# Kernel tuning notes

Hardware: AMD Instinct MI355X
Metric: run time of the kernel (lower is better)

Reference implementation:

```python
import jax, jax.numpy as jnp
import numpy as np
import math

NH, DH, BS, LOCAL, RAND, NCLS = 12, 64, 49, 3, 3, 1
WINDOW = (8, 14, 14)
NKV = LOCAL + RAND


def make_rel_pos_index():
    ws = WINDOW
    rel_size = [2 * w - 1 for w in ws]
    coords = np.stack(np.meshgrid(*[np.arange(w) for w in ws], indexing='ij')).reshape(len(ws), -1)
    rel = (coords[:, :, None] - coords[:, None, :]).transpose(1, 2, 0).astype(np.int64)
    for i, w in enumerate(ws):
        rel[:, :, i] += w - 1
    for i, r in enumerate(rel_size[1:]):
        rel[:, :, :i + 1] *= r
    n = coords.shape[1]
    S = n + NCLS
    idx = np.zeros((S, S), dtype=np.int64)
    idx[NCLS:, NCLS:] = rel.sum(-1)
    start = int(np.prod(rel_size))
    idx[:NCLS, NCLS:] = np.arange(NCLS)[:, None] + start
    start += NCLS
    idx[NCLS:, :NCLS] = np.arange(NCLS)[None, :] + start
    start += NCLS
    idx[:NCLS, :NCLS] = np.arange(NCLS ** 2).reshape(NCLS, NCLS) + start
    return idx.astype(np.int32)


def setup_inputs() -> dict:
    key = jax.random.key(0)
    ks = jax.random.split(key, 8)
    B, S, D = 8, 1569, 768
    M = (S - NCLS) // BS  # 32 blocks
    hidden_states = jax.random.normal(ks[0], (B, S, D), dtype=jnp.float32)
    Wq = jax.random.normal(ks[1], (D, D), dtype=jnp.float32) * 0.02
    bq = jax.random.normal(ks[2], (D,), dtype=jnp.float32) * 0.02
    Wk = jax.random.normal(ks[3], (D, D), dtype=jnp.float32) * 0.02
    Wv = jax.random.normal(ks[4], (D, D), dtype=jnp.float32) * 0.02
    bv = jax.random.normal(ks[5], (D,), dtype=jnp.float32) * 0.02
    rel_table = jax.random.normal(ks[6], (10938, NH), dtype=jnp.float32) * 0.02
    rel_pos_index = jnp.asarray(make_rel_pos_index())
    rand_idx = jnp.sort(jax.random.randint(ks[7], (M, RAND), 0, M), axis=1).astype(jnp.int32)
    return {"hidden_states": hidden_states, "Wq": Wq, "bq": bq, "Wk": Wk, "Wv": Wv,
            "bv": bv, "rel_table": rel_table, "rel_pos_index": rel_pos_index, "rand_idx": rand_idx}


def reference(hidden_states, Wq, bq, Wk, Wv, bv, rel_table, rel_pos_index, rand_idx):
    B, S, D = hidden_states.shape
    scale = 1.0 / math.sqrt(DH)
    q = hidden_states @ Wq + bq
    k = hidden_states @ Wk          # key has no bias in BeitSelfAttention
    v = hidden_states @ Wv + bv
    split = lambda x: x.reshape(B, S, NH, DH).transpose(0, 2, 1, 3)  # b h s d
    q, k, v = split(q), split(k), split(v)

    # --- dense attention for cls queries over all keys ---
    cls_q = q[:, :, :NCLS]
    sim_cls = jnp.einsum('bhid,bhjd->bhij', cls_q, k) * scale
    bias_cls = rel_table[rel_pos_index[:NCLS, :]]           # [ncls, S, H]
    sim_cls = sim_cls + bias_cls.transpose(2, 0, 1)[None]
    attn_cls = jax.nn.softmax(sim_cls, axis=-1)
    out_cls = jnp.einsum('bhij,bhjd->bhid', attn_cls, v)    # [B,H,ncls,DH]

    # --- block-sparse attention for local queries ---
    loc_q = q[:, :, NCLS:]
    cls_k, loc_k = k[:, :, :NCLS], k[:, :, NCLS:]
    cls_v, loc_v = v[:, :, :NCLS], v[:, :, NCLS:]
    N = S - NCLS
    M = N // BS  # evenly divisible -> pad_q = 0
    qb = loc_q.reshape(B, NH, M, BS, DH)
    kb = loc_k.reshape(B, NH, M, BS, DH)
    vb = loc_v.reshape(B, NH, M, BS, DH)

    # local + random key-block indices per query block: [M, NKV]
    offs = jnp.arange(-(LOCAL // 2), LOCAL // 2 + 1)
    local_idx = (jnp.arange(M)[:, None] + offs[None, :]) % M
    attn_idx = jnp.concatenate([local_idx.astype(jnp.int32), rand_idx], axis=1)

    kg = kb[:, :, attn_idx]   # [B,H,M,NKV,BS,DH]
    vg = vb[:, :, attn_idx]

    sim_loc = jnp.einsum('bhmid,bhmnjd->bhminj', qb, kg).reshape(B, NH, M, BS, NKV * BS)
    sim_c = jnp.einsum('bhmid,bhjd->bhmij', qb, cls_k)       # [B,H,M,BS,ncls]
    sim = jnp.concatenate([sim_c, sim_loc], axis=-1) * scale

    # gathered relative-position bias: query tokens are ncls..S-1 in order
    key_tok = (NCLS + attn_idx[:, :, None] * BS + jnp.arange(BS)[None, None, :]).reshape(M, NKV * BS)
    to_idx = jnp.concatenate([jnp.broadcast_to(jnp.arange(NCLS)[None], (M, NCLS)), key_tok], axis=1)
    q_rows = rel_pos_index[NCLS:].reshape(M, BS, S)
    bias_idx = jnp.take_along_axis(q_rows, jnp.broadcast_to(to_idx[:, None, :], (M, BS, to_idx.shape[1])), axis=-1)
    bias = rel_table[bias_idx]                                # [M,BS,ncls+NKV*BS,H]
    sim = sim + bias.transpose(3, 0, 1, 2)[None]

    attn = jax.nn.softmax(sim, axis=-1)
    a_cls = attn[..., :NCLS]
    a_loc = attn[..., NCLS:].reshape(B, NH, M, BS, NKV, BS)
    out_loc = jnp.einsum('bhminj,bhmnjd->bhmid', a_loc, vg) \
            + jnp.einsum('bhmic,bhcd->bhmid', a_cls, cls_v)
    out_loc = out_loc.reshape(B, NH, N, DH)

    out = jnp.concatenate([out_cls, out_loc], axis=2)         # [B,H,S,DH]
    return out.transpose(0, 2, 1, 3).reshape(B, S, D)
```

## Files before the change

kernel.cpp:

```cpp
#include <hip/hip_runtime.h>


#define S_TOT   1569
#define NBATCH  8

__global__ __launch_bounds__(256) void gemm_f32(const float* __restrict__ hs,
                                                const float* __restrict__ Wq,
                                                const float* __restrict__ Wk,
                                                const float* __restrict__ Wv,
                                                const float* __restrict__ bq,
                                                const float* __restrict__ bv,
                                                float* __restrict__ Q,
                                                float* __restrict__ K,
                                                float* __restrict__ V,
                                                int b0, int nTok) {
    __shared__ float As[128][20];
    __shared__ float Bs[16][136];
    int tid = threadIdx.x;
    int t0 = blockIdx.x * 128;
    int n0 = blockIdx.y * 128;
    int which = n0 / 768;
    int ng0 = n0 - which * 768;
    const float* W = (which == 0) ? Wq : (which == 1 ? Wk : Wv);
    const float* Xb = hs + (size_t)b0 * S_TOT * 768;

    int tr = tid >> 4;
    int tc = tid & 15;

    int sat = tid >> 2;
    int sak = (tid & 3) * 4;
    int sbk = tid >> 4;
    int sbn = (tid & 15) * 8;

    float acc[8][8];
#pragma unroll
    for (int i = 0; i < 8; i++)
#pragma unroll
        for (int j = 0; j < 8; j++) acc[i][j] = 0.f;

    for (int k0 = 0; k0 < 768; k0 += 16) {
#pragma unroll
        for (int hh = 0; hh < 2; hh++) {
            int t = t0 + sat + hh * 64;
            float4 xv = make_float4(0.f, 0.f, 0.f, 0.f);
            if (t < nTok)
                xv = *(const float4*)(Xb + (size_t)t * 768 + k0 + sak);
            *(float4*)&As[sat + hh * 64][sak] = xv;
        }
        {
            const float* wr_ = W + (size_t)(k0 + sbk) * 768 + ng0 + sbn;
            *(float4*)&Bs[sbk][sbn]     = *(const float4*)(wr_);
            *(float4*)&Bs[sbk][sbn + 4] = *(const float4*)(wr_ + 4);
        }
        __syncthreads();

#pragma unroll
        for (int kq = 0; kq < 4; kq++) {
            float4 xa[8];
#pragma unroll
            for (int i = 0; i < 8; i++)
                xa[i] = *(const float4*)&As[tr * 8 + i][kq * 4];
#pragma unroll
            for (int kk = 0; kk < 4; kk++) {
                int k = kq * 4 + kk;
                float4 w0 = *(const float4*)&Bs[k][tc * 4];
                float4 w1 = *(const float4*)&Bs[k][64 + tc * 4];
#pragma unroll
                for (int i = 0; i < 8; i++) {
                    float a = (kk == 0) ? xa[i].x : (kk == 1) ? xa[i].y
                            : (kk == 2) ? xa[i].z : xa[i].w;
                    acc[i][0] = fmaf(a, w0.x, acc[i][0]);
                    acc[i][1] = fmaf(a, w0.y, acc[i][1]);
                    acc[i][2] = fmaf(a, w0.z, acc[i][2]);
                    acc[i][3] = fmaf(a, w0.w, acc[i][3]);
                    acc[i][4] = fmaf(a, w1.x, acc[i][4]);
                    acc[i][5] = fmaf(a, w1.y, acc[i][5]);
                    acc[i][6] = fmaf(a, w1.z, acc[i][6]);
                    acc[i][7] = fmaf(a, w1.w, acc[i][7]);
                }
            }
        }
        __syncthreads();
    }

    float* dst = (which == 0) ? Q : (which == 1 ? K : V);
    const float* bias = (which == 0) ? bq : (which == 2 ? bv : nullptr);
#pragma unroll
    for (int hh = 0; hh < 2; hh++) {
        int nn = ng0 + hh * 64 + tc * 4;
        int h = nn >> 6, d = nn & 63;
        float4 bv4 = make_float4(0.f, 0.f, 0.f, 0.f);
        if (bias) bv4 = *(const float4*)(bias + nn);
#pragma unroll
        for (int i = 0; i < 8; i++) {
            int t = t0 + tr * 8 + i;
            if (t >= nTok) continue;
            int bl = t / S_TOT;
            int s = t - bl * S_TOT;
            float4 o;
            o.x = acc[i][hh * 4 + 0] + bv4.x;
            o.y = acc[i][hh * 4 + 1] + bv4.y;
            o.z = acc[i][hh * 4 + 2] + bv4.z;
            o.w = acc[i][hh * 4 + 3] + bv4.w;
            *(float4*)(dst + ((size_t)(bl * 12 + h) * S_TOT + s) * 64 + d) = o;
        }
    }
}

__global__ __launch_bounds__(256) void cls_attn(const float* __restrict__ Q,
                                                const float* __restrict__ K,
                                                const float* __restrict__ V,
                                                const float* __restrict__ rel,
                                                const int* __restrict__ rpi,
                                                float* __restrict__ out, int b0) {
    int bh = blockIdx.x;
    int bl = bh / 12, h = bh - bl * 12;
    __shared__ float p[S_TOT];
    __shared__ float4 qs4[16];
    __shared__ float red[256];
    __shared__ float wred[8];
    int tid = threadIdx.x, lane = tid & 63, w = tid >> 6;
    size_t base = (size_t)bh * S_TOT * 64;
    const float* Qb = Q + base;
    const float* Kb = K + base;
    const float* Vb = V + base;
    if (tid < 64) ((float*)qs4)[tid] = Qb[tid];
    __syncthreads();

    float lmx = -1e30f;
    for (int j = tid; j < S_TOT; j += 256) {
        const float4* kr = (const float4*)(Kb + j * 64);
        float a = 0.f;
#pragma unroll
        for (int d4 = 0; d4 < 16; d4++) {
            float4 kv = kr[d4];
            float4 qv = qs4[d4];
            a = fmaf(qv.x, kv.x, a); a = fmaf(qv.y, kv.y, a);
            a = fmaf(qv.z, kv.z, a); a = fmaf(qv.w, kv.w, a);
        }
        a = a * 0.125f + rel[rpi[j] * 12 + h];
        p[j] = a;
        lmx = fmaxf(lmx, a);
    }
#pragma unroll
    for (int off = 32; off > 0; off >>= 1) lmx = fmaxf(lmx, __shfl_xor(lmx, off));
    if (lane == 0) wred[w] = lmx;
    __syncthreads();
    float mx = fmaxf(fmaxf(wred[0], wred[1]), fmaxf(wred[2], wred[3]));
    float lsum = 0.f;
    for (int j = tid; j < S_TOT; j += 256) {
        float e = __expf(p[j] - mx);
        p[j] = e;
        lsum += e;
    }
#pragma unroll
    for (int off = 32; off > 0; off >>= 1) lsum += __shfl_xor(lsum, off);
    if (lane == 0) wred[4 + w] = lsum;
    __syncthreads();
    float inv = 1.0f / (wred[4] + wred[5] + wred[6] + wred[7]);
    float acc = 0.f;
    for (int j = w; j < S_TOT; j += 4) acc = fmaf(p[j], Vb[j * 64 + lane], acc);
    red[w * 64 + lane] = acc;
    __syncthreads();
    if (w == 0) {
        float o = (red[lane] + red[64 + lane] + red[128 + lane] + red[192 + lane]) * inv;
        out[(size_t)(b0 + bl) * S_TOT * 768 + h * 64 + lane] = o;
    }
}

__global__ __launch_bounds__(256, 4) void loc_attn(const float* __restrict__ Q,
                                                   const float* __restrict__ K,
                                                   const float* __restrict__ V,
                                                   const float* __restrict__ rel,
                                                   const int* __restrict__ rpi,
                                                   const int* __restrict__ rand_idx,
                                                   float* __restrict__ out, int b0) {
    int m = blockIdx.x;
    int h = blockIdx.y;
    int bl = blockIdx.z;
    __shared__ float Qlds[52][64];
    __shared__ float Plds[4][13][64];
    __shared__ int   tok[320];
    int tid = threadIdx.x, lane = tid & 63, w = tid >> 6;

    size_t base = (size_t)((bl * 12 + h) * S_TOT) * 64;
    const float* Qb = Q + base;
    const float* Kb = K + base;
    const float* Vb = V + base;

    for (int jj = tid; jj < 320; jj += 256) {
        int t = 0;
        if (jj >= 1 && jj < 295) {
            int j1 = jj - 1;
            int n = j1 / 49;
            int q = j1 - n * 49;
            int a;
            if (n == 0)      a = (m + 31) & 31;
            else if (n == 1) a = m;
            else if (n == 2) a = (m + 1) & 31;
            else             a = rand_idx[m * 3 + (n - 3)];
            t = 1 + a * 49 + q;
        }
        tok[jj] = t;
    }
    for (int idx = tid; idx < 52 * 64; idx += 256) {
        int r = idx >> 6, c = idx & 63;
        float qv = 0.f;
        if (r < 49) qv = Qb[(size_t)(1 + m * 49 + r) * 64 + c];
        ((float*)Qlds)[idx] = qv;
    }
    __syncthreads();

    float fm[13], fl[13], facc[13];
#pragma unroll
    for (int r = 0; r < 13; r++) { fm[r] = -1e30f; fl[r] = 0.f; facc[r] = 0.f; }

    for (int jc = 0; jc < 5; jc++) {
        int j = jc * 64 + lane;
        int tj = tok[j];
        const float* kp = Kb + (size_t)tj * 64;

        float s[13];
#pragma unroll
        for (int r = 0; r < 13; r++) s[r] = 0.f;
#pragma unroll 4
        for (int d4 = 0; d4 < 16; d4++) {
            float4 kv = *(const float4*)(kp + d4 * 4);
#pragma unroll
            for (int r = 0; r < 13; r++) {
                float4 qv = *(const float4*)&Qlds[w + 4 * r][d4 * 4];
                s[r] = fmaf(qv.x, kv.x, s[r]);
                s[r] = fmaf(qv.y, kv.y, s[r]);
                s[r] = fmaf(qv.z, kv.z, s[r]);
                s[r] = fmaf(qv.w, kv.w, s[r]);
            }
        }

        bool jv = j < 295;
#pragma unroll
        for (int r = 0; r < 13; r++) {
            int i = w + 4 * r;
            int qr = 1 + m * 49 + i;
            if (qr > S_TOT - 1) qr = S_TOT - 1;
            float sv = jv ? fmaf(s[r], 0.125f, rel[rpi[(size_t)qr * S_TOT + tj] * 12 + h])
                          : -1e30f;
            float mx = sv;
#pragma unroll
            for (int off = 32; off > 0; off >>= 1) mx = fmaxf(mx, __shfl_xor(mx, off));
            float mnew = fmaxf(fm[r], mx);
            float p = __expf(sv - mnew);
            float alpha = __expf(fm[r] - mnew);
            fm[r] = mnew;
            float ps = p;
#pragma unroll
            for (int off = 32; off > 0; off >>= 1) ps += __shfl_xor(ps, off);
            fl[r] = fmaf(fl[r], alpha, ps);
            facc[r] *= alpha;
            Plds[w][r][lane] = p;
        }

#pragma unroll 4
        for (int jg = 0; jg < 16; jg++) {
            int jb = jc * 64 + jg * 4;
            int t0 = tok[jb + 0], t1 = tok[jb + 1], t2 = tok[jb + 2], t3 = tok[jb + 3];
            float v0 = Vb[(size_t)t0 * 64 + lane];
            float v1 = Vb[(size_t)t1 * 64 + lane];
            float v2 = Vb[(size_t)t2 * 64 + lane];
            float v3 = Vb[(size_t)t3 * 64 + lane];
#pragma unroll
            for (int r = 0; r < 13; r++) {
                float4 p4 = *(const float4*)&Plds[w][r][jg * 4];
                facc[r] = fmaf(p4.x, v0, facc[r]);
                facc[r] = fmaf(p4.y, v1, facc[r]);
                facc[r] = fmaf(p4.z, v2, facc[r]);
                facc[r] = fmaf(p4.w, v3, facc[r]);
            }
        }
    }

    int nrows = (w == 0) ? 13 : 12;
    for (int r = 0; r < nrows; r++) {
        int i = w + 4 * r;
        int st = 1 + m * 49 + i;
        out[((size_t)(b0 + bl) * S_TOT + st) * 768 + h * 64 + lane] = facc[r] / fl[r];
    }
}

extern "C" void kernel_launch(void* const* d_in, const int* in_sizes, int n_in,
                              void* d_out, int out_size, void* d_ws, size_t ws_size,
                              hipStream_t stream) {
    (void)in_sizes; (void)n_in; (void)out_size;
    const float* hs  = (const float*)d_in[0];
    const float* Wq  = (const float*)d_in[1];
    const float* bq  = (const float*)d_in[2];
    const float* Wk  = (const float*)d_in[3];
    const float* Wv  = (const float*)d_in[4];
    const float* bv  = (const float*)d_in[5];
    const float* rel = (const float*)d_in[6];
    const int*   rpi = (const int*)d_in[7];
    const int*   rnd = (const int*)d_in[8];
    float* out = (float*)d_out;
    char* ws = (char*)d_ws;

    constexpr size_t PBUF = (size_t)12 * S_TOT * 64 * 4;

    int C = 1;
    if (ws_size >= 3 * PBUF) {
        size_t c = ws_size / (3 * PBUF);
        C = (c >= NBATCH) ? NBATCH : (int)c;
        if (C < 1) C = 1;
    }
    float* Q = (float*)(ws);
    float* K = (float*)(ws + (size_t)C * PBUF);
    float* V = (float*)(ws + (size_t)C * PBUF * 2);

    for (int b0 = 0; b0 < NBATCH; b0 += C) {
        int cb = (NBATCH - b0 < C) ? (NBATCH - b0) : C;
        int nTok = cb * S_TOT;
        gemm_f32<<<dim3((nTok + 127) / 128, 18), dim3(256), 0, stream>>>(
            hs, Wq, Wk, Wv, bq, bv, Q, K, V, b0, nTok);
        cls_attn<<<dim3(12 * cb), dim3(256), 0, stream>>>(Q, K, V, rel, rpi, out, b0);
        loc_attn<<<dim3(32, 12, cb), dim3(256), 0, stream>>>(Q, K, V, rel, rpi, rnd, out, b0);
    }
}
```

Measured before the change: 1.246 ms.

## Compute relative-position bias index analytically and remap loc_attn blocks per XCD

The local attention kernel no longer reads the large S×S relative-position index table. It derives the bias index from the 3D coordinates (z, y, x) of the query and key tokens, and uses a fixed index for the CLS column. The grid is also flattened and remapped so that consecutive blocks of the same batch/head group land on the same XCD, which should improve L2 reuse of K and V. The cost is integer division work per key and per query row, and a formula tied to the fixed window shape.

```diff
diff --git a/kernel.cpp b/kernel.cpp
--- a/kernel.cpp
+++ b/kernel.cpp
@@ -172,12 +172,17 @@
                                                    const float* __restrict__ K,
                                                    const float* __restrict__ V,
                                                    const float* __restrict__ rel,
-                                                   const int* __restrict__ rpi,
                                                    const int* __restrict__ rand_idx,
-                                                   float* __restrict__ out, int b0) {
-    int m = blockIdx.x;
-    int h = blockIdx.y;
-    int bl = blockIdx.z;
+                                                   float* __restrict__ out,
+                                                   int b0, int ng) {
+    int d = blockIdx.x;
+    int xcd = d & 7, kk_ = d >> 3;
+    int slot = xcd * (ng << 2) + kk_;
+    int g = slot >> 5;
+    int m = slot & 31;
+    int h = g % 12;
+    int bl = g / 12;
+
     __shared__ float Qlds[52][64];
     __shared__ float Plds[4][13][64];
     __shared__ int   tok[320];
@@ -211,6 +216,20 @@
     }
     __syncthreads();
 
+    int cq[13];
+#pragma unroll
+    for (int r = 0; r < 13; r++) {
+        int i = w + 4 * r;
+        int qr = 1 + m * 49 + i;
+        if (qr > S_TOT - 1) qr = S_TOT - 1;
+        int pq = qr - 1;
+        int zq = pq / 196;
+        int rem = pq - zq * 196;
+        int yq = rem / 14;
+        int xq = rem - yq * 14;
+        cq[r] = zq * 729 + yq * 27 + xq;
+    }
+
     float fm[13], fl[13], facc[13];
 #pragma unroll
     for (int r = 0; r < 13; r++) { fm[r] = -1e30f; fl[r] = 0.f; facc[r] = 0.f; }
@@ -219,6 +238,14 @@
         int j = jc * 64 + lane;
         int tj = tok[j];
         const float* kp = Kb + (size_t)tj * 64;
+
+        int pj = tj - 1;
+        int zj = pj / 196;
+        int remj = pj - zj * 196;
+        int yj = remj / 14;
+        int xj = remj - yj * 14;
+        int cj = zj * 729 + yj * 27 + xj;
+        bool iscls = (tj == 0);
 
         float s[13];
 #pragma unroll
@@ -239,10 +266,8 @@
         bool jv = j < 295;
 #pragma unroll
         for (int r = 0; r < 13; r++) {
-            int i = w + 4 * r;
-            int qr = 1 + m * 49 + i;
-            if (qr > S_TOT - 1) qr = S_TOT - 1;
-            float sv = jv ? fmaf(s[r], 0.125f, rel[rpi[(size_t)qr * S_TOT + tj] * 12 + h])
+            int bidx = iscls ? 10936 : (cq[r] - cj + 5467);
+            float sv = jv ? fmaf(s[r], 0.125f, rel[bidx * 12 + h])
                           : -1e30f;
             float mx = sv;
 #pragma unroll
@@ -320,6 +345,8 @@
         gemm_f32<<<dim3((nTok + 127) / 128, 18), dim3(256), 0, stream>>>(
             hs, Wq, Wk, Wv, bq, bv, Q, K, V, b0, nTok);
         cls_attn<<<dim3(12 * cb), dim3(256), 0, stream>>>(Q, K, V, rel, rpi, out, b0);
-        loc_attn<<<dim3(32, 12, cb), dim3(256), 0, stream>>>(Q, K, V, rel, rpi, rnd, out, b0);
+        int ngrp = 12 * cb;
+        loc_attn<<<dim3(32 * ngrp), dim3(256), 0, stream>>>(
+            Q, K, V, rel, rnd, out, b0, ngrp);
     }
 }
```

After: 1.202 ms. -3.5%, faster.
